# Kernel optimization log

Hardware: AMD Instinct MI355X
Metric: run time of the kernel (lower is better)

The kernel has to match this reference:

```python
import jax, jax.numpy as jnp
import numpy as np

N, D, H, O, E = 50000, 512, 512, 256, 150000
NEG_SLOPE = 0.2
EPS = 1e-16


def gat_conv(x, edge_index, W_src, W_dst, a_src, a_dst, bias):
    """Single-head PyG GATConv, add_self_loops=False.
    x: [N, Din]; edge_index: [2, E] (row 0 = src, row 1 = dst).
    W_src/W_dst: [Din, C]; a_src/a_dst: [C]; bias: [C].
    """
    src, dst = edge_index[0], edge_index[1]
    h_src = x @ W_src                      # [N, C]
    h_dst = x @ W_dst                      # [N, C]
    alpha_src = h_src @ a_src              # [N]
    alpha_dst = h_dst @ a_dst              # [N]
    e = jax.nn.leaky_relu(alpha_src[src] + alpha_dst[dst], NEG_SLOPE)  # [E]
    # per-destination segment softmax (numerically stable)
    m = jax.ops.segment_max(e, dst, num_segments=N)       # [N]
    ex = jnp.exp(e - m[dst])                               # [E]
    s = jax.ops.segment_sum(ex, dst, num_segments=N)       # [N]
    alpha = ex / (s[dst] + EPS)                            # [E]
    # scatter-add weighted source messages to destinations
    out = jax.ops.segment_sum(alpha[:, None] * h_src[src], dst, num_segments=N)  # [N, C]
    return out + bias


def setup_inputs() -> dict:
    key = jax.random.key(0)
    ks = jax.random.split(key, 20)
    g = lambda i, shape, sc: (jax.random.normal(ks[i], shape, dtype=jnp.float32) * sc)
    inp = {
        "x": jax.random.normal(ks[0], (N, D), dtype=jnp.float32),
        "edge_index": jax.random.randint(ks[1], (2, E), 0, N, dtype=jnp.int32),
        "edge_index_2_hop": jax.random.randint(ks[2], (2, E), 0, N, dtype=jnp.int32),
        # conv1 (D -> H)
        "W1_src": g(3, (D, H), 0.05), "W1_dst": g(4, (D, H), 0.05),
        "a1_src": g(5, (H,), 0.05), "a1_dst": g(6, (H,), 0.05),
        "b1": jnp.zeros((H,), jnp.float32),
        # lin1 (H -> H)
        "Wl1": g(7, (H, H), 0.05), "bl1": jnp.zeros((H,), jnp.float32),
        # conv2 (H -> O)
        "W2_src": g(8, (H, O), 0.05), "W2_dst": g(9, (H, O), 0.05),
        "a2_src": g(10, (O,), 0.05), "a2_dst": g(11, (O,), 0.05),
        "b2": jnp.zeros((O,), jnp.float32),
        # lin2 (O -> O)
        "Wl2": g(12, (O, O), 0.05), "bl2": jnp.zeros((O,), jnp.float32),
    }
    return inp


def reference(x, edge_index, edge_index_2_hop,
              W1_src, W1_dst, a1_src, a1_dst, b1, Wl1, bl1,
              W2_src, W2_dst, a2_src, a2_dst, b2, Wl2, bl2):
    h = (gat_conv(x, edge_index, W1_src, W1_dst, a1_src, a1_dst, b1)
         + gat_conv(x, edge_index_2_hop, W1_src, W1_dst, a1_src, a1_dst, b1))
    h = jax.nn.relu(h @ Wl1 + bl1)
    h = (gat_conv(h, edge_index, W2_src, W2_dst, a2_src, a2_dst, b2)
         + gat_conv(h, edge_index_2_hop, W2_src, W2_dst, a2_src, a2_dst, b2))
    return h @ Wl2 + bl2
```

## Files before the change

kernel.cpp:

```cpp
#include <hip/hip_runtime.h>

typedef unsigned short u16;
typedef __attribute__((ext_vector_type(8))) unsigned short v8u16;
typedef __attribute__((ext_vector_type(4))) unsigned short v4u16;
typedef __attribute__((ext_vector_type(8))) __bf16 v8bf;
typedef __attribute__((ext_vector_type(4))) float v4f;

#define NN 50000
#define EE 150000
#define SCAN_CHUNK 512
#define NB_PER_SET 98

__device__ inline float b2f(u16 u) {
    union { unsigned int i; float f; } x; x.i = ((unsigned int)u) << 16; return x.f;
}
__device__ inline u16 f2b(float f) {
    union { float f; unsigned int i; } x; x.f = f;
    unsigned int r = x.i + 0x7FFFu + ((x.i >> 16) & 1u);
    return (u16)(r >> 16);
}
__device__ inline float wred(float v) {
    v += __shfl_down(v, 32, 64);
    v += __shfl_down(v, 16, 64);
    v += __shfl_down(v, 8, 64);
    v += __shfl_down(v, 4, 64);
    v += __shfl_down(v, 2, 64);
    v += __shfl_down(v, 1, 64);
    return v;
}
__device__ inline int wred_i(int v) {
    v += __shfl_down(v, 32, 64);
    v += __shfl_down(v, 16, 64);
    v += __shfl_down(v, 8, 64);
    v += __shfl_down(v, 4, 64);
    v += __shfl_down(v, 2, 64);
    v += __shfl_down(v, 1, 64);
    return v;
}


__global__ void transpose4(const float* __restrict__ W0, u16* __restrict__ T0,
                           const float* __restrict__ W1, u16* __restrict__ T1,
                           const float* __restrict__ W2, u16* __restrict__ T2,
                           const float* __restrict__ W3, u16* __restrict__ T3) {
    int idx = blockIdx.x * blockDim.x + threadIdx.x;
    const float* W; u16* T; int N, K, base;
    if (idx < 262144)      { W = W0; T = T0; K = 512; N = 512; base = 0; }
    else if (idx < 524288) { W = W1; T = T1; K = 512; N = 512; base = 262144; }
    else if (idx < 655360) { W = W2; T = T2; K = 512; N = 256; base = 524288; }
    else if (idx < 720896) { W = W3; T = T3; K = 256; N = 256; base = 655360; }
    else return;
    int i = idx - base;
    int n = i % N, k = i / N;
    T[(size_t)n * K + k] = f2b(W[i]);
}

__global__ void wv4(const float* __restrict__ Wa, const float* __restrict__ Wb,
                    const float* __restrict__ Wc, const float* __restrict__ Wd,
                    const float* __restrict__ aa, const float* __restrict__ ab,
                    const float* __restrict__ ac, const float* __restrict__ ad,
                    float* __restrict__ vbuf) {
    int rw = (blockIdx.x * blockDim.x + threadIdx.x) >> 6;
    int lane = threadIdx.x & 63;
    if (rw >= 2048) return;
    int seg = rw >> 9, r = rw & 511;
    const float* W; const float* a; int C;
    if (seg == 0)      { W = Wa; a = aa; C = 512; }
    else if (seg == 1) { W = Wb; a = ab; C = 512; }
    else if (seg == 2) { W = Wc; a = ac; C = 256; }
    else               { W = Wd; a = ad; C = 256; }
    float s = 0.f;
    int c0 = lane * 8;
    if (c0 < C) {
        const float* wp = W + (size_t)r * C + c0;
        v4f w0 = *(const v4f*)wp;
        v4f w1 = *(const v4f*)(wp + 4);
        v4f a0 = *(const v4f*)(a + c0);
        v4f a1 = *(const v4f*)(a + c0 + 4);
#pragma unroll
        for (int j = 0; j < 4; ++j) s += w0[j] * a0[j] + w1[j] * a1[j];
    }
    s = wred(s);
    if (lane == 0) vbuf[rw] = s;
}

__global__ void alpha_pair_f32x(const float* __restrict__ X, const float* __restrict__ vs,
                                const float* __restrict__ vd, float* __restrict__ as_,
                                float* __restrict__ ad_, u16* __restrict__ Xb, int Nn) {
    int w = (blockIdx.x * blockDim.x + threadIdx.x) >> 6;
    int lane = threadIdx.x & 63;
    if (w >= Nn) return;
    const float* xp = X + (size_t)w * 512 + lane * 8;
    v4f x0 = *(const v4f*)xp;
    v4f x1 = *(const v4f*)(xp + 4);
    const float* vsp = vs + lane * 8;
    const float* vdp = vd + lane * 8;
    float s1 = 0.f, s2 = 0.f;
    v8u16 o;
#pragma unroll
    for (int j = 0; j < 4; ++j) {
        s1 += x0[j] * vsp[j] + x1[j] * vsp[j + 4];
        s2 += x0[j] * vdp[j] + x1[j] * vdp[j + 4];
        o[j] = f2b(x0[j]); o[j + 4] = f2b(x1[j]);
    }
    *(v8u16*)(Xb + (size_t)w * 512 + lane * 8) = o;
    s1 = wred(s1);
    s2 = wred(s2);
    if (lane == 0) { as_[w] = s1; ad_[w] = s2; }
}

__global__ void alpha_pair_bf16(const u16* __restrict__ X, const float* __restrict__ vs,
                                const float* __restrict__ vd, float* __restrict__ as_,
                                float* __restrict__ ad_, int Nn) {
    int w = (blockIdx.x * blockDim.x + threadIdx.x) >> 6;
    int lane = threadIdx.x & 63;
    if (w >= Nn) return;
    v8u16 xv = *(const v8u16*)(X + (size_t)w * 512 + lane * 8);
    const float* vsp = vs + lane * 8;
    const float* vdp = vd + lane * 8;
    float s1 = 0.f, s2 = 0.f;
#pragma unroll
    for (int j = 0; j < 8; ++j) {
        float xf = b2f(xv[j]);
        s1 += xf * vsp[j];
        s2 += xf * vdp[j];
    }
    s1 = wred(s1);
    s2 = wred(s2);
    if (lane == 0) { as_[w] = s1; ad_[w] = s2; }
}


__global__ void deg2_kernel(const int* __restrict__ ei1, const int* __restrict__ ei2,
                            int* __restrict__ deg) {
    int idx = blockIdx.x * blockDim.x + threadIdx.x;
    if (idx >= 2 * EE) return;
    int set = idx >= EE;
    int e = idx - set * EE;
    const int* ei = set ? ei2 : ei1;
    atomicAdd(&deg[set * NN + ei[EE + e]], 1);
}

__global__ void scan_partial(const int* __restrict__ deg, int* __restrict__ bsum) {
    int b = blockIdx.x;
    int set = b / NB_PER_SET, lb = b - set * NB_PER_SET;
    int tid = threadIdx.x;
    int i0 = lb * SCAN_CHUNK + tid * 2;
    int s = 0;
    if (i0 < NN)     s += deg[set * NN + i0];
    if (i0 + 1 < NN) s += deg[set * NN + i0 + 1];
    s = wred_i(s);
    __shared__ int lsum[4];
    if ((tid & 63) == 0) lsum[tid >> 6] = s;
    __syncthreads();
    if (tid == 0) bsum[b] = lsum[0] + lsum[1] + lsum[2] + lsum[3];
}

__global__ void scan_tops(int* __restrict__ bsum) {
    __shared__ int ls[256];
    int tid = threadIdx.x;
    int set = tid >> 7, lb = tid & 127;
    int v = (lb < NB_PER_SET) ? bsum[set * NB_PER_SET + lb] : 0;
    ls[tid] = v;
    __syncthreads();
    for (int off = 1; off < 128; off <<= 1) {
        int t = (lb >= off) ? ls[tid - off] : 0;
        __syncthreads();
        ls[tid] += t;
        __syncthreads();
    }
    if (lb < NB_PER_SET) bsum[set * NB_PER_SET + lb] = ls[tid] - v;
}

__global__ void scan_final(const int* __restrict__ deg, const int* __restrict__ bsum,
                           int* __restrict__ rp) {
    int b = blockIdx.x;
    int set = b / NB_PER_SET, lb = b - set * NB_PER_SET;
    int tid = threadIdx.x;
    int i0 = lb * SCAN_CHUNK + tid * 2;
    int d0 = (i0 < NN)     ? deg[set * NN + i0]     : 0;
    int d1 = (i0 + 1 < NN) ? deg[set * NN + i0 + 1] : 0;
    int pair = d0 + d1;
    __shared__ int ps[256];
    ps[tid] = pair;
    __syncthreads();
    for (int off = 1; off < 256; off <<= 1) {
        int t = (tid >= off) ? ps[tid - off] : 0;
        __syncthreads();
        ps[tid] += t;
        __syncthreads();
    }
    int base = bsum[b] + ps[tid] - pair;
    if (i0 < NN)     rp[set * (NN + 1) + i0] = base;
    if (i0 + 1 < NN) rp[set * (NN + 1) + i0 + 1] = base + d0;
    if (b == 0 && tid == 0) { rp[NN] = EE; rp[(NN + 1) + NN] = EE; }
}

__global__ void fill2_kernel(const int* __restrict__ ei1, const int* __restrict__ ei2,
                             const int* __restrict__ rp, int* __restrict__ deg,
                             int* __restrict__ srcp, int* __restrict__ dstp) {
    int idx = blockIdx.x * blockDim.x + threadIdx.x;
    if (idx >= 2 * EE) return;
    int set = idx >= EE;
    int e = idx - set * EE;
    const int* ei = set ? ei2 : ei1;
    int d = ei[EE + e];
    int old = atomicSub(&deg[set * NN + d], 1);
    int pos = rp[set * (NN + 1) + d] + old - 1;
    srcp[set * EE + pos] = ei[e];
    dstp[set * EE + pos] = d;
}

__global__ void edge_ex(const int* __restrict__ srcp, const int* __restrict__ dstp,
                        const float* __restrict__ asrc, const float* __restrict__ adst,
                        float* __restrict__ ex) {
    int i = blockIdx.x * blockDim.x + threadIdx.x;
    if (i >= 2 * EE) return;
    float t = asrc[srcp[i]] + adst[dstp[i]];
    t = t > 0.f ? t : 0.2f * t;
    ex[i] = __expf(fminf(t, 60.f));
}

template <int CV>
__global__ void gat_pull(const int* __restrict__ rp, const int* __restrict__ srcp,
                         const float* __restrict__ ex, const u16* __restrict__ H,
                         const float* __restrict__ bias, u16* __restrict__ G, int Nn) {
    const int C = CV * 64;
    int d = (blockIdx.x * blockDim.x + threadIdx.x) >> 6;
    int lane = threadIdx.x & 63;
    if (d >= Nn) return;
    float out[CV];
#pragma unroll
    for (int j = 0; j < CV; ++j) out[j] = 0.f;
#pragma unroll
    for (int set = 0; set < 2; ++set) {
        const int* rpS = rp + set * (NN + 1);
        int base = set * EE;
        int beg = rpS[d], end = rpS[d + 1];
        float acc[CV];
#pragma unroll
        for (int j = 0; j < CV; ++j) acc[j] = 0.f;
        float ssum = 0.f;
        for (int i = beg; i < end; ++i) {
            float w = ex[base + i];
            int s = srcp[base + i];
            ssum += w;
            const u16* hp = H + (size_t)s * C + lane * CV;
            if constexpr (CV == 8) {
                v8u16 hv = *(const v8u16*)hp;
#pragma unroll
                for (int j = 0; j < 8; ++j) acc[j] += w * b2f(hv[j]);
            } else {
                v4u16 hv = *(const v4u16*)hp;
#pragma unroll
                for (int j = 0; j < 4; ++j) acc[j] += w * b2f(hv[j]);
            }
        }
        float inv = 1.f / (ssum + 1e-16f);
#pragma unroll
        for (int j = 0; j < CV; ++j) out[j] += acc[j] * inv;
    }
    const float* bp = bias + lane * CV;
    u16* gp = G + (size_t)d * C + lane * CV;
    if constexpr (CV == 8) {
        v8u16 o;
#pragma unroll
        for (int j = 0; j < 8; ++j) o[j] = f2b(out[j] + 2.f * bp[j]);
        *(v8u16*)gp = o;
    } else {
        v4u16 o;
#pragma unroll
        for (int j = 0; j < 4; ++j) o[j] = f2b(out[j] + 2.f * bp[j]);
        *(v4u16*)gp = o;
    }
}

__global__ __launch_bounds__(256, 2) void gemm_bf16(
    const u16* __restrict__ A, const u16* __restrict__ Bt, void* __restrict__ Cv,
    int M, int N, int K, const float* __restrict__ bias, int relu, int outf32) {
    __shared__ u16 As[128 * 40];
    __shared__ u16 Bs[128 * 40];
    const int tid = threadIdx.x;
    const int lane = tid & 63;
    const int wid = tid >> 6;
    const int wm = wid >> 1;
    const int wn = wid & 1;
    const int quad = lane >> 4;
    const int l16 = lane & 15;
    const int tileM = blockIdx.x * 128;
    const int tileN = blockIdx.y * 128;

    v4f acc[4][4];
#pragma unroll
    for (int i = 0; i < 4; ++i)
#pragma unroll
        for (int j = 0; j < 4; ++j) acc[i][j] = v4f{0.f, 0.f, 0.f, 0.f};

    for (int k0 = 0; k0 < K; k0 += 32) {
#pragma unroll
        for (int r = 0; r < 2; ++r) {
            int idx = r * 256 + tid;
            int row = idx >> 2;
            int col = (idx & 3) << 3;
            int ga = tileM + row; ga = ga < M ? ga : M - 1;
            *(v8u16*)&As[row * 40 + col] = *(const v8u16*)(A + (size_t)ga * K + k0 + col);
            *(v8u16*)&Bs[row * 40 + col] = *(const v8u16*)(Bt + (size_t)(tileN + row) * K + k0 + col);
        }
        __syncthreads();
        v8bf af[4], bfr[4];
#pragma unroll
        for (int i = 0; i < 4; ++i)
            af[i] = __builtin_bit_cast(v8bf, *(const v8u16*)&As[(wm * 64 + i * 16 + l16) * 40 + quad * 8]);
#pragma unroll
        for (int i = 0; i < 4; ++i)
            bfr[i] = __builtin_bit_cast(v8bf, *(const v8u16*)&Bs[(wn * 64 + i * 16 + l16) * 40 + quad * 8]);
#pragma unroll
        for (int mi = 0; mi < 4; ++mi)
#pragma unroll
            for (int ni = 0; ni < 4; ++ni)
                acc[mi][ni] = __builtin_amdgcn_mfma_f32_16x16x32_bf16(af[mi], bfr[ni], acc[mi][ni], 0, 0, 0);
        __syncthreads();
    }

#pragma unroll
    for (int mi = 0; mi < 4; ++mi)
#pragma unroll
        for (int ni = 0; ni < 4; ++ni) {
            int col = tileN + wn * 64 + ni * 16 + l16;
            float bb = bias ? bias[col] : 0.f;
            int row0 = tileM + wm * 64 + mi * 16 + quad * 4;
#pragma unroll
            for (int r = 0; r < 4; ++r) {
                int row = row0 + r;
                if (row < M) {
                    float v = acc[mi][ni][r] + bb;
                    if (relu) v = fmaxf(v, 0.f);
                    if (outf32) ((float*)Cv)[(size_t)row * N + col] = v;
                    else        ((u16*)Cv)[(size_t)row * N + col] = f2b(v);
                }
            }
        }
}


extern "C" void kernel_launch(void* const* d_in, const int* in_sizes, int n_in,
                              void* d_out, int out_size, void* d_ws, size_t ws_size,
                              hipStream_t stream) {
    const float* x  = (const float*)d_in[0];
    const int* ei1  = (const int*)d_in[1];
    const int* ei2  = (const int*)d_in[2];
    const float* W1s = (const float*)d_in[3];
    const float* W1d = (const float*)d_in[4];
    const float* a1s = (const float*)d_in[5];
    const float* a1d = (const float*)d_in[6];
    const float* b1  = (const float*)d_in[7];
    const float* Wl1 = (const float*)d_in[8];
    const float* bl1 = (const float*)d_in[9];
    const float* W2s = (const float*)d_in[10];
    const float* W2d = (const float*)d_in[11];
    const float* a2s = (const float*)d_in[12];
    const float* a2d = (const float*)d_in[13];
    const float* b2  = (const float*)d_in[14];
    const float* Wl2 = (const float*)d_in[15];
    const float* bl2 = (const float*)d_in[16];
    float* out = (float*)d_out;

    char* ws = (char*)d_ws;
    size_t off = 0;
    auto alloc = [&](size_t b) { void* p = ws + off; off = (off + b + 255) & ~(size_t)255; return p; };
    u16* bufA   = (u16*)alloc((size_t)NN * 512 * 2);
    u16* bufB   = (u16*)alloc((size_t)NN * 512 * 2);
    int* rp     = (int*)alloc((size_t)2 * (NN + 1) * 4);
    int* srcp   = (int*)alloc((size_t)2 * EE * 4);
    int* dstp   = (int*)alloc((size_t)2 * EE * 4);
    int* deg    = (int*)alloc((size_t)2 * NN * 4);
    int* bsum   = (int*)alloc((size_t)2 * NB_PER_SET * 4);
    float* ex   = (float*)alloc((size_t)2 * EE * 4);
    float* asrc = (float*)alloc((size_t)NN * 4);
    float* adst = (float*)alloc((size_t)NN * 4);
    float* vbuf = (float*)alloc(2048 * 4);
    u16* Wt1s   = (u16*)alloc((size_t)512 * 512 * 2);
    u16* Wtl1   = (u16*)alloc((size_t)512 * 512 * 2);
    u16* Wt2s   = (u16*)alloc((size_t)512 * 256 * 2);
    u16* Wtl2   = (u16*)alloc((size_t)256 * 256 * 2);
    u16* g2buf  = bufB + (size_t)NN * 256;

    hipMemsetAsync(deg, 0, (size_t)2 * NN * 4, stream);
    deg2_kernel<<<(2 * EE + 255) / 256, 256, 0, stream>>>(ei1, ei2, deg);
    scan_partial<<<2 * NB_PER_SET, 256, 0, stream>>>(deg, bsum);
    scan_tops<<<1, 256, 0, stream>>>(bsum);
    scan_final<<<2 * NB_PER_SET, 256, 0, stream>>>(deg, bsum, rp);
    fill2_kernel<<<(2 * EE + 255) / 256, 256, 0, stream>>>(ei1, ei2, rp, deg, srcp, dstp);

    transpose4<<<(720896 + 255) / 256, 256, 0, stream>>>(W1s, Wt1s, Wl1, Wtl1, W2s, Wt2s, Wl2, Wtl2);
    wv4<<<512, 256, 0, stream>>>(W1s, W1d, W2s, W2d, a1s, a1d, a2s, a2d, vbuf);

    alpha_pair_f32x<<<(NN + 3) / 4, 256, 0, stream>>>(x, vbuf, vbuf + 512, asrc, adst, bufB, NN);
    edge_ex<<<(2 * EE + 255) / 256, 256, 0, stream>>>(srcp, dstp, asrc, adst, ex);
    gemm_bf16<<<dim3(391, 4), 256, 0, stream>>>(bufB, Wt1s, bufA, NN, 512, 512, nullptr, 0, 0);
    gat_pull<8><<<(NN + 3) / 4, 256, 0, stream>>>(rp, srcp, ex, bufA, b1, bufB, NN);
    gemm_bf16<<<dim3(391, 4), 256, 0, stream>>>(bufB, Wtl1, bufA, NN, 512, 512, bl1, 1, 0);

    alpha_pair_bf16<<<(NN + 3) / 4, 256, 0, stream>>>(bufA, vbuf + 1024, vbuf + 1536, asrc, adst, NN);
    edge_ex<<<(2 * EE + 255) / 256, 256, 0, stream>>>(srcp, dstp, asrc, adst, ex);
    gemm_bf16<<<dim3(391, 2), 256, 0, stream>>>(bufA, Wt2s, bufB, NN, 256, 512, nullptr, 0, 0);
    gat_pull<4><<<(NN + 3) / 4, 256, 0, stream>>>(rp, srcp, ex, bufB, b2, g2buf, NN);
    gemm_bf16<<<dim3(391, 2), 256, 0, stream>>>(g2buf, Wtl2, out, NN, 256, 256, bl2, 0, 1);

    (void)in_sizes; (void)n_in; (void)out_size; (void)ws_size;
}
```

Before: 549.4 us.

## Load GEMM tiles via global_load_lds and swap grid axes for tile reuse

The bf16 GEMM now copies its A and B tiles directly from global memory into LDS with global_load_lds 16-byte transfers, replacing register-staged loads and stores. The LDS row pitch drops from 40 to 32, which drops the padding and may cause bank conflicts on the fragment reads. The grid axes are also swapped so that blocks sharing the same M-tile run next to each other, which should improve L2 reuse of A. The direct-to-LDS path saves VGPRs and instructions, but nothing overlaps the loads with compute because the kernel still synchronises before every MFMA step.

```diff
diff --git a/kernel.cpp b/kernel.cpp
--- a/kernel.cpp
+++ b/kernel.cpp
@@ -36,6 +36,12 @@
     v += __shfl_down(v, 2, 64);
     v += __shfl_down(v, 1, 64);
     return v;
+}
+
+__device__ __forceinline__ void gll16(const u16* g, u16* l) {
+    __builtin_amdgcn_global_load_lds(
+        (const __attribute__((address_space(1))) void*)g,
+        (__attribute__((address_space(3))) void*)l, 16, 0, 0);
 }
 
 
@@ -278,8 +284,8 @@
 __global__ __launch_bounds__(256, 2) void gemm_bf16(
     const u16* __restrict__ A, const u16* __restrict__ Bt, void* __restrict__ Cv,
     int M, int N, int K, const float* __restrict__ bias, int relu, int outf32) {
-    __shared__ u16 As[128 * 40];
-    __shared__ u16 Bs[128 * 40];
+    __shared__ u16 As[128 * 32];
+    __shared__ u16 Bs[128 * 32];
     const int tid = threadIdx.x;
     const int lane = tid & 63;
     const int wid = tid >> 6;
@@ -287,8 +293,21 @@
     const int wn = wid & 1;
     const int quad = lane >> 4;
     const int l16 = lane & 15;
-    const int tileM = blockIdx.x * 128;
-    const int tileN = blockIdx.y * 128;
+    const int tileM = blockIdx.y * 128;
+    const int tileN = blockIdx.x * 128;
+
+    const int srow = tid >> 2;
+    const int scol = (tid & 3) * 8;
+    int ra0 = tileM + srow;       if (ra0 >= M) ra0 = M - 1;
+    int ra1 = tileM + 64 + srow;  if (ra1 >= M) ra1 = M - 1;
+    const u16* gA0 = A + (size_t)ra0 * K + scol;
+    const u16* gA1 = A + (size_t)ra1 * K + scol;
+    const u16* gB0 = Bt + (size_t)(tileN + srow) * K + scol;
+    const u16* gB1 = Bt + (size_t)(tileN + 64 + srow) * K + scol;
+    u16* lA0 = As + wid * 512;
+    u16* lA1 = As + 2048 + wid * 512;
+    u16* lB0 = Bs + wid * 512;
+    u16* lB1 = Bs + 2048 + wid * 512;
 
     v4f acc[4][4];
 #pragma unroll
@@ -297,23 +316,18 @@
         for (int j = 0; j < 4; ++j) acc[i][j] = v4f{0.f, 0.f, 0.f, 0.f};
 
     for (int k0 = 0; k0 < K; k0 += 32) {
-#pragma unroll
-        for (int r = 0; r < 2; ++r) {
-            int idx = r * 256 + tid;
-            int row = idx >> 2;
-            int col = (idx & 3) << 3;
-            int ga = tileM + row; ga = ga < M ? ga : M - 1;
-            *(v8u16*)&As[row * 40 + col] = *(const v8u16*)(A + (size_t)ga * K + k0 + col);
-            *(v8u16*)&Bs[row * 40 + col] = *(const v8u16*)(Bt + (size_t)(tileN + row) * K + k0 + col);
-        }
+        gll16(gA0 + k0, lA0);
+        gll16(gA1 + k0, lA1);
+        gll16(gB0 + k0, lB0);
+        gll16(gB1 + k0, lB1);
         __syncthreads();
         v8bf af[4], bfr[4];
 #pragma unroll
         for (int i = 0; i < 4; ++i)
-            af[i] = __builtin_bit_cast(v8bf, *(const v8u16*)&As[(wm * 64 + i * 16 + l16) * 40 + quad * 8]);
+            af[i] = __builtin_bit_cast(v8bf, *(const v8u16*)&As[(wm * 64 + i * 16 + l16) * 32 + quad * 8]);
 #pragma unroll
         for (int i = 0; i < 4; ++i)
-            bfr[i] = __builtin_bit_cast(v8bf, *(const v8u16*)&Bs[(wn * 64 + i * 16 + l16) * 40 + quad * 8]);
+            bfr[i] = __builtin_bit_cast(v8bf, *(const v8u16*)&Bs[(wn * 64 + i * 16 + l16) * 32 + quad * 8]);
 #pragma unroll
         for (int mi = 0; mi < 4; ++mi)
 #pragma unroll
@@ -397,15 +411,15 @@
 
     alpha_pair_f32x<<<(NN + 3) / 4, 256, 0, stream>>>(x, vbuf, vbuf + 512, asrc, adst, bufB, NN);
     edge_ex<<<(2 * EE + 255) / 256, 256, 0, stream>>>(srcp, dstp, asrc, adst, ex);
-    gemm_bf16<<<dim3(391, 4), 256, 0, stream>>>(bufB, Wt1s, bufA, NN, 512, 512, nullptr, 0, 0);
+    gemm_bf16<<<dim3(4, 391), 256, 0, stream>>>(bufB, Wt1s, bufA, NN, 512, 512, nullptr, 0, 0);
     gat_pull<8><<<(NN + 3) / 4, 256, 0, stream>>>(rp, srcp, ex, bufA, b1, bufB, NN);
-    gemm_bf16<<<dim3(391, 4), 256, 0, stream>>>(bufB, Wtl1, bufA, NN, 512, 512, bl1, 1, 0);
+    gemm_bf16<<<dim3(4, 391), 256, 0, stream>>>(bufB, Wtl1, bufA, NN, 512, 512, bl1, 1, 0);
 
     alpha_pair_bf16<<<(NN + 3) / 4, 256, 0, stream>>>(bufA, vbuf + 1024, vbuf + 1536, asrc, adst, NN);
     edge_ex<<<(2 * EE + 255) / 256, 256, 0, stream>>>(srcp, dstp, asrc, adst, ex);
-    gemm_bf16<<<dim3(391, 2), 256, 0, stream>>>(bufA, Wt2s, bufB, NN, 256, 512, nullptr, 0, 0);
+    gemm_bf16<<<dim3(2, 391), 256, 0, stream>>>(bufA, Wt2s, bufB, NN, 256, 512, nullptr, 0, 0);
     gat_pull<4><<<(NN + 3) / 4, 256, 0, stream>>>(rp, srcp, ex, bufB, b2, g2buf, NN);
-    gemm_bf16<<<dim3(391, 2), 256, 0, stream>>>(g2buf, Wtl2, out, NN, 256, 256, bl2, 0, 1);
+    gemm_bf16<<<dim3(2, 391), 256, 0, stream>>>(g2buf, Wtl2, out, NN, 256, 256, bl2, 0, 1);
 
     (void)in_sizes; (void)n_in; (void)out_size; (void)ws_size;
 }
```

Result: faster. 537.9 us (-2.1%).
